# Performance work log

Hardware: AMD Instinct MI355X
Metric: run time of the kernel (lower is better)

## Reference

```python
import jax, jax.numpy as jnp
import numpy as np

NATOMS = 50000          # edge_vector rows
M = 3 * NATOMS          # attention nodes = numel(edge_vector)
NE = 1500000            # edges
NH, DH = 4, 16          # num_heads, head dim (out_dim // num_heads)


def _glorot(key, shape):
    fan_in, fan_out = shape
    lim = (6.0 / (fan_in + fan_out)) ** 0.5
    return jax.random.uniform(key, shape, jnp.float32, -lim, lim)


def setup_inputs() -> dict:
    key = jax.random.key(0)
    ks = jax.random.split(key, 12)
    inp = {
        "node_attr": jax.random.normal(ks[0], (2, M), jnp.float32),
        "edge_index": jax.random.randint(ks[1], (2, NE), 0, M, jnp.int64),
        "edge_feature": jax.random.normal(ks[2], (NE, 4), jnp.float32),
        "edge_vector": jax.random.normal(ks[3], (NATOMS, 3), jnp.float32),
        # parameters (hardcoded layer sizes in the torch module)
        "W1": _glorot(ks[4], (1, 4)),   "b1": jnp.zeros((4,), jnp.float32),
        "W2": _glorot(ks[5], (4, 16)),  "b2": jnp.zeros((16,), jnp.float32),
        "W": _glorot(ks[6], (16, 64)),  "b": jnp.zeros((64,), jnp.float32),
        "Wout": _glorot(ks[7], (64, 16)), "bout": jnp.zeros((16,), jnp.float32),
        "Wout1": _glorot(ks[8], (16, 1)), "bout1": jnp.zeros((1,), jnp.float32),
    }
    return inp


def reference(node_attr, edge_index, edge_feature, edge_vector,
              W1, b1, W2, b2, W, b, Wout, bout, Wout1, bout1):
    # node pathway: each scalar of edge_vector is one attention node
    h = edge_vector.reshape(-1, 1)                      # [M, 1]
    h = jax.nn.elu(h @ W1 + b1)                         # [M, 4]  (dropout = identity, eval)
    h = (h @ W2 + b2).reshape(-1, DH)                   # [M, 16]
    qkv = (h @ W + b).reshape(-1, NH, DH)               # [M, 4, 16]; Q==K==V (shared linear)

    # edge pathway
    e = jax.nn.elu(edge_feature @ W2 + b2)              # [Ne, 16]
    E = (e @ W + b).reshape(-1, NH, DH)                 # [Ne, 4, 16]

    src_idx = edge_index[0]
    dst_idx = edge_index[1]
    src = qkv[src_idx]                                  # K_h gather [Ne,4,16]
    dst = qkv[dst_idx]                                  # Q_h gather [Ne,4,16]
    score = (src * dst) * (1.0 / np.sqrt(DH)) * E       # edge-conditioned scores
    score = jnp.exp(jnp.clip(score.sum(-1, keepdims=True), -5.0, 5.0))  # [Ne,4,1]

    msg = qkv[src_idx] * score                          # V_h gather * score
    wV = jax.ops.segment_sum(msg, dst_idx, num_segments=M)      # [M,4,16]
    Z = jax.ops.segment_sum(score, dst_idx, num_segments=M)     # [M,4,1]

    h_out = (wV / (Z + 1e-6)).reshape(-1, NH * DH)      # [M, 64]
    h_out = jax.nn.elu(h_out @ Wout + bout)             # [M, 16]
    h_out = (h_out @ Wout1 + bout1).reshape(-1, 3)      # [M/3, 3]
    return h_out
```

## Files before the change

kernel.cpp:

```cpp
#include <hip/hip_runtime.h>
#include <hip/hip_bf16.h>
#include <cstdint>

#define DEVI __device__ __forceinline__

typedef __attribute__((ext_vector_type(8))) short bf16x8;
typedef __attribute__((ext_vector_type(4))) float f32x4;

DEVI float bf2f(unsigned short u) {
    union { unsigned int i; float f; } v; v.i = ((unsigned int)u) << 16; return v.f;
}
DEVI float ldf(const void* p, long long i, int f32) {
    return f32 ? ((const float*)p)[i] : bf2f(((const unsigned short*)p)[i]);
}
DEVI unsigned short f2bfu(float x) {
    __hip_bfloat16 h = __float2bfloat16(x);
    return *reinterpret_cast<unsigned short*>(&h);
}
DEVI short f2bf(float x) { return (short)f2bfu(x); }
DEVI float eluf(float x) { return x > 0.f ? x : __expf(x) - 1.f; }

__global__ __launch_bounds__(64) void detect_k(
    const int* __restrict__ eidx32, const unsigned int* __restrict__ wbits,
    int* __restrict__ flags)
{
    int t = threadIdx.x;
    int odd = eidx32[2 * t + 1];
    unsigned long long bz = __ballot(odd == 0);
    unsigned int w = wbits[t];
    unsigned int ex = (w >> 23) & 0xFF;
    unsigned long long bf = __ballot(ex >= 100 && ex <= 130);
    if (t == 0) {
        flags[0] = (bz == ~0ULL) ? 1 : 0;
        flags[1] = (__popcll(bf) >= 48) ? 1 : 0;
    }
}

__global__ __launch_bounds__(256) void node_qkv_k(
    const int* __restrict__ flags,
    const void* __restrict__ evec,
    const void* __restrict__ W1, const void* __restrict__ b1,
    const void* __restrict__ W2, const void* __restrict__ b2,
    const void* __restrict__ W,  const void* __restrict__ b,
    unsigned short* __restrict__ qkvb, int M_)
{
    __shared__ float sW[1024], sW2[64], sb[64], sb2[16], sW1[4], sb1[4];
    int t = threadIdx.x;
    int f32 = flags[1];
    for (int i = t; i < 1024; i += 256) sW[i] = ldf(W, i, f32);
    if (t < 64) { sW2[t] = ldf(W2, t, f32); sb[t] = ldf(b, t, f32); }
    if (t < 16) sb2[t] = ldf(b2, t, f32);
    if (t < 4)  { sW1[t] = ldf(W1, t, f32); sb1[t] = ldf(b1, t, f32); }
    __syncthreads();

    int m = blockIdx.x * 256 + t;
    if (m >= M_) return;

    float x = ldf(evec, m, f32);
    float h1[4];
    #pragma unroll
    for (int j = 0; j < 4; ++j) h1[j] = eluf(fmaf(x, sW1[j], sb1[j]));
    float h2[16];
    #pragma unroll
    for (int k = 0; k < 16; ++k) h2[k] = sb2[k];
    #pragma unroll
    for (int j = 0; j < 4; ++j)
        #pragma unroll
        for (int k = 0; k < 16; ++k) h2[k] = fmaf(h1[j], sW2[j*16 + k], h2[k]);

    uint4* op = (uint4*)(qkvb + (size_t)m * 64);
    for (int g = 0; g < 8; ++g) {
        float v[8];
        #pragma unroll
        for (int j = 0; j < 8; ++j) {
            int c = g * 8 + j;
            float a = sb[c];
            #pragma unroll
            for (int k = 0; k < 16; ++k) a = fmaf(h2[k], sW[k*64 + c], a);
            v[j] = a;
        }
        uint4 pk;
        pk.x = (unsigned)f2bfu(v[0]) | ((unsigned)f2bfu(v[1]) << 16);
        pk.y = (unsigned)f2bfu(v[2]) | ((unsigned)f2bfu(v[3]) << 16);
        pk.z = (unsigned)f2bfu(v[4]) | ((unsigned)f2bfu(v[5]) << 16);
        pk.w = (unsigned)f2bfu(v[6]) | ((unsigned)f2bfu(v[7]) << 16);
        op[g] = pk;
    }
}

__global__ __launch_bounds__(256) void hist_k(
    const int* __restrict__ flags, const int* __restrict__ eidx32,
    int* __restrict__ counts, int NE_)
{
    int e = blockIdx.x * 256 + threadIdx.x;
    if (e >= NE_) return;
    int i64 = flags[0];
    int dst = i64 ? eidx32[2LL * (NE_ + (long long)e)] : eidx32[(long long)NE_ + e];
    atomicAdd(&counts[dst], 1);
}

__global__ __launch_bounds__(256) void scan_a_k(
    const int* __restrict__ counts, int* __restrict__ bsum, int M_)
{
    __shared__ int s[256];
    int t = threadIdx.x;
    int g4 = blockIdx.x * 256 + t;
    int i0 = g4 * 4;
    int v = 0;
    if (i0 + 3 < M_) {
        int4 c = ((const int4*)counts)[g4];
        v = c.x + c.y + c.z + c.w;
    } else {
        for (int k = 0; k < 4 && i0 + k < M_; ++k) v += counts[i0 + k];
    }
    s[t] = v; __syncthreads();
    for (int off = 128; off > 0; off >>= 1) {
        if (t < off) s[t] += s[t + off];
        __syncthreads();
    }
    if (t == 0) bsum[blockIdx.x] = s[0];
}

__global__ __launch_bounds__(256) void scan_b_k(
    const int* __restrict__ bsum, int* __restrict__ bexcl, int nb,
    int* __restrict__ offsets, int M_, int NE_)
{
    __shared__ int s[256];
    int t = threadIdx.x;
    int mine = (t < nb) ? bsum[t] : 0;
    s[t] = mine; __syncthreads();
    for (int off = 1; off < 256; off <<= 1) {
        int v = (t >= off) ? s[t - off] : 0;
        __syncthreads();
        s[t] += v;
        __syncthreads();
    }
    if (t < nb) bexcl[t] = s[t] - mine;
    if (t == 0) offsets[M_] = NE_;
}

__global__ __launch_bounds__(256) void scan_c_k(
    const int* __restrict__ counts, const int* __restrict__ bexcl,
    int* __restrict__ offsets, int* __restrict__ cursor, int M_)
{
    __shared__ int s[256];
    int t = threadIdx.x;
    int g4 = blockIdx.x * 256 + t;
    int i0 = g4 * 4;
    int c0 = 0, c1 = 0, c2 = 0, c3 = 0;
    if (i0 + 3 < M_) {
        int4 c = ((const int4*)counts)[g4];
        c0 = c.x; c1 = c.y; c2 = c.z; c3 = c.w;
    } else {
        if (i0 + 0 < M_) c0 = counts[i0 + 0];
        if (i0 + 1 < M_) c1 = counts[i0 + 1];
        if (i0 + 2 < M_) c2 = counts[i0 + 2];
        if (i0 + 3 < M_) c3 = counts[i0 + 3];
    }
    int tsum = c0 + c1 + c2 + c3;
    s[t] = tsum; __syncthreads();
    for (int off = 1; off < 256; off <<= 1) {
        int v = (t >= off) ? s[t - off] : 0;
        __syncthreads();
        s[t] += v;
        __syncthreads();
    }
    int run = bexcl[blockIdx.x] + s[t] - tsum;
    if (i0 + 0 < M_) { offsets[i0+0] = run; cursor[i0+0] = run; run += c0; }
    if (i0 + 1 < M_) { offsets[i0+1] = run; cursor[i0+1] = run; run += c1; }
    if (i0 + 2 < M_) { offsets[i0+2] = run; cursor[i0+2] = run; run += c2; }
    if (i0 + 3 < M_) { offsets[i0+3] = run; cursor[i0+3] = run; run += c3; }
}

__global__ __launch_bounds__(256) void scatter_k(
    const int* __restrict__ flags, const int* __restrict__ eidx32,
    const void* __restrict__ efeat,
    int* __restrict__ cursor, int4* __restrict__ sorted, int NE_)
{
    int e = blockIdx.x * 256 + threadIdx.x;
    if (e >= NE_) return;
    int i64 = flags[0];
    int f32 = flags[1];
    int src, dst;
    if (i64) { src = eidx32[2LL * e]; dst = eidx32[2LL * (NE_ + (long long)e)]; }
    else     { src = eidx32[e];       dst = eidx32[(long long)NE_ + e]; }

    unsigned int ef01, ef23;
    if (f32) {
        const float4 f = ((const float4*)efeat)[e];
        ef01 = (unsigned)f2bfu(f.x) | ((unsigned)f2bfu(f.y) << 16);
        ef23 = (unsigned)f2bfu(f.z) | ((unsigned)f2bfu(f.w) << 16);
    } else {
        const uint2 u = ((const uint2*)efeat)[e];
        ef01 = u.x; ef23 = u.y;
    }

    int pos = atomicAdd(&cursor[dst], 1);
    sorted[pos] = make_int4(src, dst, (int)ef01, (int)ef23);
}

__global__ __launch_bounds__(256) void score_k(
    const int* __restrict__ flags, const int4* __restrict__ sorted,
    const void* __restrict__ W2, const void* __restrict__ b2,
    const void* __restrict__ W,  const void* __restrict__ b,
    const unsigned short* __restrict__ qkvb, float* __restrict__ score, int NE_)
{
    __shared__ float sW2[64], sb2[16];
    __shared__ float sE[4][16 * 68];
    int t = threadIdx.x;
    int f32 = flags[1];
    if (t < 64) sW2[t] = ldf(W2, t, f32);
    if (t < 16) sb2[t] = ldf(b2, t, f32);
    __syncthreads();

    int wv   = t >> 6;
    int lane = t & 63;
    int col  = lane & 15;
    int quad = lane >> 4;
    float* myE = &sE[wv][0];

    bf16x8 bfrag[4];
    float  bb[4];
    #pragma unroll
    for (int h = 0; h < 4; ++h) {
        #pragma unroll
        for (int jj = 0; jj < 8; ++jj) {
            int k = quad * 8 + jj;
            float wv_ = (k < 16) ? ldf(W, k * 64 + h * 16 + col, f32) : 0.f;
            bfrag[h][jj] = f2bf(wv_);
        }
        bb[h] = ldf(b, h * 16 + col, f32);
    }

    int j2 = lane >> 2, h2 = lane & 3;

    long long tiles = ((long long)NE_ + 15) >> 4;
    long long wid   = (long long)blockIdx.x * 4 + wv;
    long long nw    = (long long)gridDim.x * 4;

    for (long long tile = wid; tile < tiles; tile += nw) {
        int base = (int)(tile << 4);

        int jA = base + col;
        int4 rec = make_int4(0, 0, 0, 0);
        if (jA < NE_) rec = sorted[jA];
        float ef0 = bf2f((unsigned short)((unsigned)rec.z & 0xffff));
        float ef1 = bf2f((unsigned short)((unsigned)rec.z >> 16));
        float ef2 = bf2f((unsigned short)((unsigned)rec.w & 0xffff));
        float ef3 = bf2f((unsigned short)((unsigned)rec.w >> 16));

        bf16x8 afrag;
        #pragma unroll
        for (int jj = 0; jj < 8; ++jj) {
            int k = quad * 8 + jj;
            float v = 0.f;
            if (k < 16) {
                v = eluf(fmaf(ef0, sW2[k],
                        fmaf(ef1, sW2[16 + k],
                        fmaf(ef2, sW2[32 + k],
                        fmaf(ef3, sW2[48 + k], sb2[k])))));
            }
            afrag[jj] = f2bf(v);
        }

        f32x4 acc[4];
        #pragma unroll
        for (int h = 0; h < 4; ++h) {
            acc[h] = (f32x4){0.f, 0.f, 0.f, 0.f};
            acc[h] = __builtin_amdgcn_mfma_f32_16x16x32_bf16(afrag, bfrag[h], acc[h], 0, 0, 0);
        }

        #pragma unroll
        for (int h = 0; h < 4; ++h)
            #pragma unroll
            for (int r = 0; r < 4; ++r)
                myE[(quad * 4 + r) * 68 + h * 16 + col] = acc[h][r] + bb[h];

        asm volatile("s_waitcnt lgkmcnt(0)" ::: "memory");

        int srcj = __shfl(rec.x, j2, 64);
        int dstj = __shfl(rec.y, j2, 64);

        const uint4* sp = (const uint4*)(qkvb + (size_t)srcj * 64 + h2 * 16);
        const uint4* dp = (const uint4*)(qkvb + (size_t)dstj * 64 + h2 * 16);
        uint4 sA = sp[0], sB = sp[1], dA = dp[0], dB = dp[1];

        const float4* ep = (const float4*)(myE + j2 * 68 + h2 * 16);
        float4 e0 = ep[0], e1 = ep[1], e2 = ep[2], e3 = ep[3];
        float E[16] = {e0.x,e0.y,e0.z,e0.w, e1.x,e1.y,e1.z,e1.w,
                       e2.x,e2.y,e2.z,e2.w, e3.x,e3.y,e3.z,e3.w};

        unsigned int su[8] = {sA.x,sA.y,sA.z,sA.w, sB.x,sB.y,sB.z,sB.w};
        unsigned int du[8] = {dA.x,dA.y,dA.z,dA.w, dB.x,dB.y,dB.z,dB.w};

        float sc = 0.f;
        #pragma unroll
        for (int i = 0; i < 8; ++i) {
            float s0 = bf2f((unsigned short)(su[i] & 0xffff));
            float s1 = bf2f((unsigned short)(su[i] >> 16));
            float d0 = bf2f((unsigned short)(du[i] & 0xffff));
            float d1 = bf2f((unsigned short)(du[i] >> 16));
            sc = fmaf(s0 * d0, E[2*i],   sc);
            sc = fmaf(s1 * d1, E[2*i+1], sc);
        }
        sc *= 0.25f;
        sc = fminf(fmaxf(sc, -5.f), 5.f);
        float s = __expf(sc);

        int jW = base + j2;
        if (jW < NE_) score[(size_t)jW * 4 + h2] = s;
    }
}

__global__ __launch_bounds__(256) void accum_out_k(
    const int* __restrict__ flags,
    const int* __restrict__ offsets, const int4* __restrict__ sorted,
    const float* __restrict__ score, const unsigned short* __restrict__ qkvb,
    const void* __restrict__ Wout, const void* __restrict__ bout,
    const void* __restrict__ Wout1, const void* __restrict__ bout1,
    void* __restrict__ out, int M_)
{
    __shared__ float sWo[1024], sbo[16], sWo1[16];
    __shared__ float sbo1;
    int t = threadIdx.x;
    int f32 = flags[1];
    for (int i = t; i < 1024; i += 256) sWo[i] = ldf(Wout, i, f32);
    if (t < 16) { sbo[t] = ldf(bout, t, f32); sWo1[t] = ldf(Wout1, t, f32); }
    if (t == 0) sbo1 = ldf(bout1, 0, f32);
    __syncthreads();

    int gid = blockIdx.x * 256 + t;
    int m = gid >> 2;
    if (m >= M_) return;
    int h  = gid & 3;
    int hb = h * 16;

    int beg = offsets[m], end = offsets[m + 1];

    float acc[16];
    #pragma unroll
    for (int d = 0; d < 16; ++d) acc[d] = 0.f;
    float z = 0.f;

    int j = beg;
    for (; j + 2 <= end; j += 2) {
        int s0 = sorted[j].x;
        int s1 = sorted[j + 1].x;
        float sc0 = score[(size_t)j * 4 + h];
        float sc1 = score[(size_t)(j + 1) * 4 + h];
        const uint4* p0 = (const uint4*)(qkvb + (size_t)s0 * 64 + hb);
        const uint4* p1 = (const uint4*)(qkvb + (size_t)s1 * 64 + hb);
        uint4 a0 = p0[0], a1 = p0[1];
        uint4 b0 = p1[0], b1 = p1[1];
        z += sc0 + sc1;
        unsigned int q0[8] = {a0.x,a0.y,a0.z,a0.w, a1.x,a1.y,a1.z,a1.w};
        unsigned int q1[8] = {b0.x,b0.y,b0.z,b0.w, b1.x,b1.y,b1.z,b1.w};
        #pragma unroll
        for (int i = 0; i < 8; ++i) {
            acc[2*i]   = fmaf(bf2f((unsigned short)(q0[i] & 0xffff)), sc0, acc[2*i]);
            acc[2*i+1] = fmaf(bf2f((unsigned short)(q0[i] >> 16)),    sc0, acc[2*i+1]);
        }
        #pragma unroll
        for (int i = 0; i < 8; ++i) {
            acc[2*i]   = fmaf(bf2f((unsigned short)(q1[i] & 0xffff)), sc1, acc[2*i]);
            acc[2*i+1] = fmaf(bf2f((unsigned short)(q1[i] >> 16)),    sc1, acc[2*i+1]);
        }
    }
    if (j < end) {
        int s0 = sorted[j].x;
        float sc0 = score[(size_t)j * 4 + h];
        const uint4* p0 = (const uint4*)(qkvb + (size_t)s0 * 64 + hb);
        uint4 a0 = p0[0], a1 = p0[1];
        z += sc0;
        unsigned int q0[8] = {a0.x,a0.y,a0.z,a0.w, a1.x,a1.y,a1.z,a1.w};
        #pragma unroll
        for (int i = 0; i < 8; ++i) {
            acc[2*i]   = fmaf(bf2f((unsigned short)(q0[i] & 0xffff)), sc0, acc[2*i]);
            acc[2*i+1] = fmaf(bf2f((unsigned short)(q0[i] >> 16)),    sc0, acc[2*i+1]);
        }
    }

    float zinv = 1.f / (z + 1e-6f);

    float p[16];
    #pragma unroll
    for (int jj = 0; jj < 16; ++jj) p[jj] = 0.f;
    #pragma unroll
    for (int d = 0; d < 16; ++d) {
        float hv = acc[d] * zinv;
        #pragma unroll
        for (int jj = 0; jj < 16; ++jj) p[jj] = fmaf(hv, sWo[(hb + d) * 16 + jj], p[jj]);
    }
    #pragma unroll
    for (int jj = 0; jj < 16; ++jj) {
        p[jj] += __shfl_xor(p[jj], 1, 64);
        p[jj] += __shfl_xor(p[jj], 2, 64);
    }
    if (h == 0) {
        float o = sbo1;
        #pragma unroll
        for (int jj = 0; jj < 16; ++jj) o = fmaf(eluf(p[jj] + sbo[jj]), sWo1[jj], o);
        if (f32) ((float*)out)[m] = o;
        else     ((__hip_bfloat16*)out)[m] = __float2bfloat16(o);
    }
}

extern "C" void kernel_launch(void* const* d_in, const int* in_sizes, int n_in,
                              void* d_out, int out_size, void* d_ws, size_t ws_size,
                              hipStream_t stream)
{
    const int*  eidx  = (const int*)d_in[1];
    const void* efeat = d_in[2];
    const void* evec  = d_in[3];
    const void* W1 = d_in[4],  *b1 = d_in[5];
    const void* W2 = d_in[6],  *b2 = d_in[7];
    const void* W  = d_in[8],  *b  = d_in[9];
    const void* Wout = d_in[10], *bout = d_in[11];
    const void* Wout1 = d_in[12], *bout1 = d_in[13];

    const int M_  = in_sizes[3];
    const int NE_ = in_sizes[1] / 2;
    const int nb  = (M_ + 1023) / 1024;

    char* wp = (char*)d_ws;
    int*            flags   = (int*)wp;                 wp += 16;
    unsigned short* qkvb    = (unsigned short*)wp;      wp += (size_t)M_ * 64 * 2;
    int*            counts  = (int*)wp;                 wp += (size_t)M_ * 4;
    int*            bsum    = (int*)wp;                 wp += 2048 * 4;
    int*            bexcl   = (int*)wp;                 wp += 2048 * 4;
    int*            offsets = (int*)wp;                 wp += ((size_t)M_ + 4) * 4;
    int*            cursor  = (int*)wp;                 wp += ((size_t)M_ + 4) * 4;
    int4*           sorted  = (int4*)wp;                wp += (size_t)NE_ * 16;
    float*          scoreB  = (float*)wp;

    detect_k<<<1, 64, 0, stream>>>(eidx, (const unsigned int*)W, flags);
    hipMemsetAsync(counts, 0, (size_t)M_ * 4, stream);

    node_qkv_k<<<(M_ + 255) / 256, 256, 0, stream>>>(
        flags, evec, W1, b1, W2, b2, W, b, qkvb, M_);

    hist_k<<<(NE_ + 255) / 256, 256, 0, stream>>>(flags, eidx, counts, NE_);
    scan_a_k<<<nb, 256, 0, stream>>>(counts, bsum, M_);
    scan_b_k<<<1, 256, 0, stream>>>(bsum, bexcl, nb, offsets, M_, NE_);
    scan_c_k<<<nb, 256, 0, stream>>>(counts, bexcl, offsets, cursor, M_);
    scatter_k<<<(NE_ + 255) / 256, 256, 0, stream>>>(
        flags, eidx, efeat, cursor, sorted, NE_);

    long long tiles = ((long long)NE_ + 15) / 16;
    int sblocks = (int)((tiles + 3) / 4);
    if (sblocks > 12288) sblocks = 12288;
    score_k<<<sblocks, 256, 0, stream>>>(
        flags, sorted, W2, b2, W, b, qkvb, scoreB, NE_);

    long long tot = (long long)M_ * 4;
    accum_out_k<<<(int)((tot + 255) / 256), 256, 0, stream>>>(
        flags, offsets, sorted, scoreB, qkvb,
        Wout, bout, Wout1, bout1, d_out, M_);
}
```

Before: 423.8 us.

## Fuse edge score computation with per-node aggregation and output MLP

Merges the score kernel and the accumulate/output kernel into one. Each wavefront owns 16 consecutive destination nodes and walks their contiguous sorted edge range in chunks of 16. Scores and source indices are staged in shared memory and consumed immediately, so the global score buffer write and read-back go away. In exchange, each wave's work depends on its nodes' degrees, which can cause load imbalance. The inner accumulation loop is also serial per edge and the shared memory footprint per block grows.

```diff
diff --git a/kernel.cpp b/kernel.cpp
--- a/kernel.cpp
+++ b/kernel.cpp
@@ -199,25 +199,38 @@
     sorted[pos] = make_int4(src, dst, (int)ef01, (int)ef23);
 }
 
-__global__ __launch_bounds__(256) void score_k(
-    const int* __restrict__ flags, const int4* __restrict__ sorted,
+__global__ __launch_bounds__(256) void fused_k(
+    const int* __restrict__ flags,
+    const int* __restrict__ offsets, const int4* __restrict__ sorted,
     const void* __restrict__ W2, const void* __restrict__ b2,
     const void* __restrict__ W,  const void* __restrict__ b,
-    const unsigned short* __restrict__ qkvb, float* __restrict__ score, int NE_)
+    const unsigned short* __restrict__ qkvb,
+    const void* __restrict__ Wout, const void* __restrict__ bout,
+    const void* __restrict__ Wout1, const void* __restrict__ bout1,
+    void* __restrict__ out, int M_)
 {
     __shared__ float sW2[64], sb2[16];
+    __shared__ float sWo[1024], sbo[16], sWo1[16];
+    __shared__ float sbo1;
     __shared__ float sE[4][16 * 68];
+    __shared__ float sS[4][64];
+    __shared__ int   sSrc[4][16];
+
     int t = threadIdx.x;
     int f32 = flags[1];
+    for (int i = t; i < 1024; i += 256) sWo[i] = ldf(Wout, i, f32);
     if (t < 64) sW2[t] = ldf(W2, t, f32);
-    if (t < 16) sb2[t] = ldf(b2, t, f32);
+    if (t < 16) { sb2[t] = ldf(b2, t, f32); sbo[t] = ldf(bout, t, f32); sWo1[t] = ldf(Wout1, t, f32); }
+    if (t == 0) sbo1 = ldf(bout1, 0, f32);
     __syncthreads();
 
-    int wv   = t >> 6;
+    int wvi  = t >> 6;
     int lane = t & 63;
     int col  = lane & 15;
     int quad = lane >> 4;
-    float* myE = &sE[wv][0];
+    float* myE  = &sE[wvi][0];
+    float* myS  = &sS[wvi][0];
+    int*   mySrc = &sSrc[wvi][0];
 
     bf16x8 bfrag[4];
     float  bb[4];
@@ -232,18 +245,26 @@
         bb[h] = ldf(b, h * 16 + col, f32);
     }
 
+    int m0 = (blockIdx.x * 4 + wvi) * 16;
+    if (m0 >= M_) return;
+    int mtop = m0 + 16; if (mtop > M_) mtop = M_;
+    int beg = offsets[m0], end = offsets[mtop];
+
     int j2 = lane >> 2, h2 = lane & 3;
-
-    long long tiles = ((long long)NE_ + 15) >> 4;
-    long long wid   = (long long)blockIdx.x * 4 + wv;
-    long long nw    = (long long)gridDim.x * 4;
-
-    for (long long tile = wid; tile < tiles; tile += nw) {
-        int base = (int)(tile << 4);
-
-        int jA = base + col;
+    int m = m0 + j2;
+    bool valid = (m < M_);
+    int sbm = valid ? offsets[m]     : 0;
+    int sem = valid ? offsets[m + 1] : 0;
+
+    float acc[16];
+    #pragma unroll
+    for (int d = 0; d < 16; ++d) acc[d] = 0.f;
+    float z = 0.f;
+
+    for (int c = beg; c < end; c += 16) {
+        int jA = c + col;
         int4 rec = make_int4(0, 0, 0, 0);
-        if (jA < NE_) rec = sorted[jA];
+        if (jA < end) rec = sorted[jA];
         float ef0 = bf2f((unsigned short)((unsigned)rec.z & 0xffff));
         float ef1 = bf2f((unsigned short)((unsigned)rec.z >> 16));
         float ef2 = bf2f((unsigned short)((unsigned)rec.w & 0xffff));
@@ -263,24 +284,23 @@
             afrag[jj] = f2bf(v);
         }
 
-        f32x4 acc[4];
+        f32x4 a4[4];
         #pragma unroll
         for (int h = 0; h < 4; ++h) {
-            acc[h] = (f32x4){0.f, 0.f, 0.f, 0.f};
-            acc[h] = __builtin_amdgcn_mfma_f32_16x16x32_bf16(afrag, bfrag[h], acc[h], 0, 0, 0);
+            a4[h] = (f32x4){0.f, 0.f, 0.f, 0.f};
+            a4[h] = __builtin_amdgcn_mfma_f32_16x16x32_bf16(afrag, bfrag[h], a4[h], 0, 0, 0);
         }
 
         #pragma unroll
         for (int h = 0; h < 4; ++h)
             #pragma unroll
             for (int r = 0; r < 4; ++r)
-                myE[(quad * 4 + r) * 68 + h * 16 + col] = acc[h][r] + bb[h];
-
+                myE[(quad * 4 + r) * 68 + h * 16 + col] = a4[h][r] + bb[h];
+        if (lane < 16) mySrc[col] = rec.x;
         asm volatile("s_waitcnt lgkmcnt(0)" ::: "memory");
 
         int srcj = __shfl(rec.x, j2, 64);
         int dstj = __shfl(rec.y, j2, 64);
-
         const uint4* sp = (const uint4*)(qkvb + (size_t)srcj * 64 + h2 * 16);
         const uint4* dp = (const uint4*)(qkvb + (size_t)dstj * 64 + h2 * 16);
         uint4 sA = sp[0], sB = sp[1], dA = dp[0], dB = dp[1];
@@ -289,7 +309,6 @@
         float4 e0 = ep[0], e1 = ep[1], e2 = ep[2], e3 = ep[3];
         float E[16] = {e0.x,e0.y,e0.z,e0.w, e1.x,e1.y,e1.z,e1.w,
                        e2.x,e2.y,e2.z,e2.w, e3.x,e3.y,e3.z,e3.w};
-
         unsigned int su[8] = {sA.x,sA.y,sA.z,sA.w, sB.x,sB.y,sB.z,sB.w};
         unsigned int du[8] = {dA.x,dA.y,dA.z,dA.w, dB.x,dB.y,dB.z,dB.w};
 
@@ -305,83 +324,30 @@
         }
         sc *= 0.25f;
         sc = fminf(fmaxf(sc, -5.f), 5.f);
-        float s = __expf(sc);
-
-        int jW = base + j2;
-        if (jW < NE_) score[(size_t)jW * 4 + h2] = s;
-    }
-}
-
-__global__ __launch_bounds__(256) void accum_out_k(
-    const int* __restrict__ flags,
-    const int* __restrict__ offsets, const int4* __restrict__ sorted,
-    const float* __restrict__ score, const unsigned short* __restrict__ qkvb,
-    const void* __restrict__ Wout, const void* __restrict__ bout,
-    const void* __restrict__ Wout1, const void* __restrict__ bout1,
-    void* __restrict__ out, int M_)
-{
-    __shared__ float sWo[1024], sbo[16], sWo1[16];
-    __shared__ float sbo1;
-    int t = threadIdx.x;
-    int f32 = flags[1];
-    for (int i = t; i < 1024; i += 256) sWo[i] = ldf(Wout, i, f32);
-    if (t < 16) { sbo[t] = ldf(bout, t, f32); sWo1[t] = ldf(Wout1, t, f32); }
-    if (t == 0) sbo1 = ldf(bout1, 0, f32);
-    __syncthreads();
-
-    int gid = blockIdx.x * 256 + t;
-    int m = gid >> 2;
-    if (m >= M_) return;
-    int h  = gid & 3;
-    int hb = h * 16;
-
-    int beg = offsets[m], end = offsets[m + 1];
-
-    float acc[16];
-    #pragma unroll
-    for (int d = 0; d < 16; ++d) acc[d] = 0.f;
-    float z = 0.f;
-
-    int j = beg;
-    for (; j + 2 <= end; j += 2) {
-        int s0 = sorted[j].x;
-        int s1 = sorted[j + 1].x;
-        float sc0 = score[(size_t)j * 4 + h];
-        float sc1 = score[(size_t)(j + 1) * 4 + h];
-        const uint4* p0 = (const uint4*)(qkvb + (size_t)s0 * 64 + hb);
-        const uint4* p1 = (const uint4*)(qkvb + (size_t)s1 * 64 + hb);
-        uint4 a0 = p0[0], a1 = p0[1];
-        uint4 b0 = p1[0], b1 = p1[1];
-        z += sc0 + sc1;
-        unsigned int q0[8] = {a0.x,a0.y,a0.z,a0.w, a1.x,a1.y,a1.z,a1.w};
-        unsigned int q1[8] = {b0.x,b0.y,b0.z,b0.w, b1.x,b1.y,b1.z,b1.w};
-        #pragma unroll
-        for (int i = 0; i < 8; ++i) {
-            acc[2*i]   = fmaf(bf2f((unsigned short)(q0[i] & 0xffff)), sc0, acc[2*i]);
-            acc[2*i+1] = fmaf(bf2f((unsigned short)(q0[i] >> 16)),    sc0, acc[2*i+1]);
-        }
-        #pragma unroll
-        for (int i = 0; i < 8; ++i) {
-            acc[2*i]   = fmaf(bf2f((unsigned short)(q1[i] & 0xffff)), sc1, acc[2*i]);
-            acc[2*i+1] = fmaf(bf2f((unsigned short)(q1[i] >> 16)),    sc1, acc[2*i+1]);
-        }
-    }
-    if (j < end) {
-        int s0 = sorted[j].x;
-        float sc0 = score[(size_t)j * 4 + h];
-        const uint4* p0 = (const uint4*)(qkvb + (size_t)s0 * 64 + hb);
-        uint4 a0 = p0[0], a1 = p0[1];
-        z += sc0;
-        unsigned int q0[8] = {a0.x,a0.y,a0.z,a0.w, a1.x,a1.y,a1.z,a1.w};
-        #pragma unroll
-        for (int i = 0; i < 8; ++i) {
-            acc[2*i]   = fmaf(bf2f((unsigned short)(q0[i] & 0xffff)), sc0, acc[2*i]);
-            acc[2*i+1] = fmaf(bf2f((unsigned short)(q0[i] >> 16)),    sc0, acc[2*i+1]);
-        }
-    }
+        myS[j2 * 4 + h2] = __expf(sc);
+        asm volatile("s_waitcnt lgkmcnt(0)" ::: "memory");
+
+        int lo = sbm - c; if (lo < 0) lo = 0;
+        int hi = sem - c; if (hi > 16) hi = 16;
+        for (int jj = lo; jj < hi; ++jj) {
+            float s = myS[jj * 4 + h2];
+            int srcm = mySrc[jj];
+            const uint4* p = (const uint4*)(qkvb + (size_t)srcm * 64 + h2 * 16);
+            uint4 a0 = p[0], a1 = p[1];
+            z += s;
+            unsigned int q[8] = {a0.x,a0.y,a0.z,a0.w, a1.x,a1.y,a1.z,a1.w};
+            #pragma unroll
+            for (int i = 0; i < 8; ++i) {
+                acc[2*i]   = fmaf(bf2f((unsigned short)(q[i] & 0xffff)), s, acc[2*i]);
+                acc[2*i+1] = fmaf(bf2f((unsigned short)(q[i] >> 16)),    s, acc[2*i+1]);
+            }
+        }
+    }
+
+    if (!valid) return;
 
     float zinv = 1.f / (z + 1e-6f);
-
+    int hb = h2 * 16;
     float p[16];
     #pragma unroll
     for (int jj = 0; jj < 16; ++jj) p[jj] = 0.f;
@@ -396,7 +362,7 @@
         p[jj] += __shfl_xor(p[jj], 1, 64);
         p[jj] += __shfl_xor(p[jj], 2, 64);
     }
-    if (h == 0) {
+    if (h2 == 0) {
         float o = sbo1;
         #pragma unroll
         for (int jj = 0; jj < 16; ++jj) o = fmaf(eluf(p[jj] + sbo[jj]), sWo1[jj], o);
@@ -430,8 +396,7 @@
     int*            bexcl   = (int*)wp;                 wp += 2048 * 4;
     int*            offsets = (int*)wp;                 wp += ((size_t)M_ + 4) * 4;
     int*            cursor  = (int*)wp;                 wp += ((size_t)M_ + 4) * 4;
-    int4*           sorted  = (int4*)wp;                wp += (size_t)NE_ * 16;
-    float*          scoreB  = (float*)wp;
+    int4*           sorted  = (int4*)wp;
 
     detect_k<<<1, 64, 0, stream>>>(eidx, (const unsigned int*)W, flags);
     hipMemsetAsync(counts, 0, (size_t)M_ * 4, stream);
@@ -446,14 +411,8 @@
     scatter_k<<<(NE_ + 255) / 256, 256, 0, stream>>>(
         flags, eidx, efeat, cursor, sorted, NE_);
 
-    long long tiles = ((long long)NE_ + 15) / 16;
-    int sblocks = (int)((tiles + 3) / 4);
-    if (sblocks > 12288) sblocks = 12288;
-    score_k<<<sblocks, 256, 0, stream>>>(
-        flags, sorted, W2, b2, W, b, qkvb, scoreB, NE_);
-
-    long long tot = (long long)M_ * 4;
-    accum_out_k<<<(int)((tot + 255) / 256), 256, 0, stream>>>(
-        flags, offsets, sorted, scoreB, qkvb,
+    int fblocks = (M_ + 63) / 64;
+    fused_k<<<fblocks, 256, 0, stream>>>(
+        flags, offsets, sorted, W2, b2, W, b, qkvb,
         Wout, bout, Wout1, bout1, d_out, M_);
 }
```

New measurement: 452.0 us. 1.07x slower.

## Split edge scatter into coarse bucket pass and local placement pass

Applied to the files above, without the earlier changes.

Replaces the single random scatter of edges by destination with two passes. The first groups edges into buckets of 128 destination nodes, using one atomic cursor per bucket. The second reads the staging array in bucket order and places each edge at its exact slot, so its writes land in a small region. The aim is better write locality and cache behaviour during the counting sort, at the cost of an extra kernel launch, an extra pass over 1.5M 16-byte records, and heavier atomic contention on the bucket cursors. The score buffer now reuses the staging memory.

```diff
diff --git a/kernel.cpp b/kernel.cpp
--- a/kernel.cpp
+++ b/kernel.cpp
@@ -172,10 +172,17 @@
     if (i0 + 3 < M_) { offsets[i0+3] = run; cursor[i0+3] = run; run += c3; }
 }
 
-__global__ __launch_bounds__(256) void scatter_k(
+__global__ __launch_bounds__(256) void binit_k(
+    const int* __restrict__ offsets, int* __restrict__ bcur, int NB)
+{
+    int b = blockIdx.x * 256 + threadIdx.x;
+    if (b < NB) bcur[b] = offsets[b * 128];
+}
+
+__global__ __launch_bounds__(256) void bucket_k(
     const int* __restrict__ flags, const int* __restrict__ eidx32,
     const void* __restrict__ efeat,
-    int* __restrict__ cursor, int4* __restrict__ sorted, int NE_)
+    int* __restrict__ bcur, int4* __restrict__ staging, int NE_)
 {
     int e = blockIdx.x * 256 + threadIdx.x;
     if (e >= NE_) return;
@@ -195,8 +202,19 @@
         ef01 = u.x; ef23 = u.y;
     }
 
-    int pos = atomicAdd(&cursor[dst], 1);
-    sorted[pos] = make_int4(src, dst, (int)ef01, (int)ef23);
+    int pos = atomicAdd(&bcur[dst >> 7], 1);
+    staging[pos] = make_int4(src, dst, (int)ef01, (int)ef23);
+}
+
+__global__ __launch_bounds__(256) void place_k(
+    const int4* __restrict__ staging, int* __restrict__ cursor,
+    int4* __restrict__ sorted, int NE_)
+{
+    int j = blockIdx.x * 256 + threadIdx.x;
+    if (j >= NE_) return;
+    int4 r = staging[j];
+    int pos = atomicAdd(&cursor[r.y], 1);
+    sorted[pos] = r;
 }
 
 __global__ __launch_bounds__(256) void score_k(
@@ -421,6 +439,7 @@
     const int M_  = in_sizes[3];
     const int NE_ = in_sizes[1] / 2;
     const int nb  = (M_ + 1023) / 1024;
+    const int NB  = (M_ + 127) / 128;
 
     char* wp = (char*)d_ws;
     int*            flags   = (int*)wp;                 wp += 16;
@@ -430,8 +449,13 @@
     int*            bexcl   = (int*)wp;                 wp += 2048 * 4;
     int*            offsets = (int*)wp;                 wp += ((size_t)M_ + 4) * 4;
     int*            cursor  = (int*)wp;                 wp += ((size_t)M_ + 4) * 4;
+    int*            bcur    = (int*)wp;                 wp += ((size_t)NB + 4) * 4;
+    wp = (char*)(((uintptr_t)wp + 15) & ~(uintptr_t)15);
     int4*           sorted  = (int4*)wp;                wp += (size_t)NE_ * 16;
+    int4*           staging = (int4*)wp;                wp += (size_t)NE_ * 16;
     float*          scoreB  = (float*)wp;
+
+    scoreB = (float*)staging;
 
     detect_k<<<1, 64, 0, stream>>>(eidx, (const unsigned int*)W, flags);
     hipMemsetAsync(counts, 0, (size_t)M_ * 4, stream);
@@ -443,8 +467,12 @@
     scan_a_k<<<nb, 256, 0, stream>>>(counts, bsum, M_);
     scan_b_k<<<1, 256, 0, stream>>>(bsum, bexcl, nb, offsets, M_, NE_);
     scan_c_k<<<nb, 256, 0, stream>>>(counts, bexcl, offsets, cursor, M_);
-    scatter_k<<<(NE_ + 255) / 256, 256, 0, stream>>>(
-        flags, eidx, efeat, cursor, sorted, NE_);
+    binit_k<<<(NB + 255) / 256, 256, 0, stream>>>(offsets, bcur, NB);
+
+    bucket_k<<<(NE_ + 255) / 256, 256, 0, stream>>>(
+        flags, eidx, efeat, bcur, staging, NE_);
+    place_k<<<(NE_ + 255) / 256, 256, 0, stream>>>(
+        staging, cursor, sorted, NE_);
 
     long long tiles = ((long long)NE_ + 15) / 16;
     int sblocks = (int)((tiles + 3) / 4);
```

Measured after the change: 655.1 us. 54.6% more time.

## Record per-edge rank in histogram to drop atomics from scatter pass

Applied to the files above, without the earlier changes.

The histogram kernel now keeps the value returned by each atomicAdd as a per-edge rank and handles four edges per thread with vectorized index loads. The scatter kernel computes each edge's position as offsets[dst] + rank, so it no longer needs a second round of atomics on a cursor array. The cursor array and its writes in the scan kernel are removed. In exchange, a new rank array of NE ints is written and read back, and the order of edges within each segment now follows the histogram pass rather than the scatter pass.

```diff
diff --git a/kernel.cpp b/kernel.cpp
--- a/kernel.cpp
+++ b/kernel.cpp
@@ -90,13 +90,33 @@
 
 __global__ __launch_bounds__(256) void hist_k(
     const int* __restrict__ flags, const int* __restrict__ eidx32,
-    int* __restrict__ counts, int NE_)
-{
-    int e = blockIdx.x * 256 + threadIdx.x;
-    if (e >= NE_) return;
+    int* __restrict__ counts, int* __restrict__ rank, int NE_)
+{
+    int e0 = (blockIdx.x * 256 + threadIdx.x) * 4;
+    if (e0 >= NE_) return;
     int i64 = flags[0];
-    int dst = i64 ? eidx32[2LL * (NE_ + (long long)e)] : eidx32[(long long)NE_ + e];
-    atomicAdd(&counts[dst], 1);
+    if (e0 + 3 < NE_) {
+        int d[4];
+        if (i64) {
+            long long w = 2LL * (NE_ + (long long)e0);
+            int4 a = *(const int4*)(eidx32 + w);
+            int4 b = *(const int4*)(eidx32 + w + 4);
+            d[0] = a.x; d[1] = a.z; d[2] = b.x; d[3] = b.z;
+        } else {
+            #pragma unroll
+            for (int i = 0; i < 4; ++i) d[i] = eidx32[(long long)NE_ + e0 + i];
+        }
+        int r[4];
+        #pragma unroll
+        for (int i = 0; i < 4; ++i) r[i] = atomicAdd(&counts[d[i]], 1);
+        *(int4*)(rank + e0) = make_int4(r[0], r[1], r[2], r[3]);
+    } else {
+        for (int e = e0; e < NE_; ++e) {
+            int dst = i64 ? eidx32[2LL * (NE_ + (long long)e)]
+                          : eidx32[(long long)NE_ + e];
+            rank[e] = atomicAdd(&counts[dst], 1);
+        }
+    }
 }
 
 __global__ __launch_bounds__(256) void scan_a_k(
@@ -141,7 +161,7 @@
 
 __global__ __launch_bounds__(256) void scan_c_k(
     const int* __restrict__ counts, const int* __restrict__ bexcl,
-    int* __restrict__ offsets, int* __restrict__ cursor, int M_)
+    int* __restrict__ offsets, int M_)
 {
     __shared__ int s[256];
     int t = threadIdx.x;
@@ -166,16 +186,17 @@
         __syncthreads();
     }
     int run = bexcl[blockIdx.x] + s[t] - tsum;
-    if (i0 + 0 < M_) { offsets[i0+0] = run; cursor[i0+0] = run; run += c0; }
-    if (i0 + 1 < M_) { offsets[i0+1] = run; cursor[i0+1] = run; run += c1; }
-    if (i0 + 2 < M_) { offsets[i0+2] = run; cursor[i0+2] = run; run += c2; }
-    if (i0 + 3 < M_) { offsets[i0+3] = run; cursor[i0+3] = run; run += c3; }
+    if (i0 + 0 < M_) { offsets[i0+0] = run; run += c0; }
+    if (i0 + 1 < M_) { offsets[i0+1] = run; run += c1; }
+    if (i0 + 2 < M_) { offsets[i0+2] = run; run += c2; }
+    if (i0 + 3 < M_) { offsets[i0+3] = run; run += c3; }
 }
 
 __global__ __launch_bounds__(256) void scatter_k(
     const int* __restrict__ flags, const int* __restrict__ eidx32,
     const void* __restrict__ efeat,
-    int* __restrict__ cursor, int4* __restrict__ sorted, int NE_)
+    const int* __restrict__ offsets, const int* __restrict__ rank,
+    int4* __restrict__ sorted, int NE_)
 {
     int e = blockIdx.x * 256 + threadIdx.x;
     if (e >= NE_) return;
@@ -195,7 +216,7 @@
         ef01 = u.x; ef23 = u.y;
     }
 
-    int pos = atomicAdd(&cursor[dst], 1);
+    int pos = offsets[dst] + rank[e];
     sorted[pos] = make_int4(src, dst, (int)ef01, (int)ef23);
 }
 
@@ -429,22 +450,24 @@
     int*            bsum    = (int*)wp;                 wp += 2048 * 4;
     int*            bexcl   = (int*)wp;                 wp += 2048 * 4;
     int*            offsets = (int*)wp;                 wp += ((size_t)M_ + 4) * 4;
-    int*            cursor  = (int*)wp;                 wp += ((size_t)M_ + 4) * 4;
+    int*            rank    = (int*)wp;                 wp += (size_t)NE_ * 4;
+    wp = (char*)(((uintptr_t)wp + 15) & ~(uintptr_t)15);
     int4*           sorted  = (int4*)wp;                wp += (size_t)NE_ * 16;
     float*          scoreB  = (float*)wp;
 
     detect_k<<<1, 64, 0, stream>>>(eidx, (const unsigned int*)W, flags);
-    hipMemsetAsync(counts, 0, (size_t)M_ * 4, stream);
+    (void)hipMemsetAsync(counts, 0, (size_t)M_ * 4, stream);
 
     node_qkv_k<<<(M_ + 255) / 256, 256, 0, stream>>>(
         flags, evec, W1, b1, W2, b2, W, b, qkvb, M_);
 
-    hist_k<<<(NE_ + 255) / 256, 256, 0, stream>>>(flags, eidx, counts, NE_);
+    int q4 = (NE_ + 3) / 4;
+    hist_k<<<(q4 + 255) / 256, 256, 0, stream>>>(flags, eidx, counts, rank, NE_);
     scan_a_k<<<nb, 256, 0, stream>>>(counts, bsum, M_);
     scan_b_k<<<1, 256, 0, stream>>>(bsum, bexcl, nb, offsets, M_, NE_);
-    scan_c_k<<<nb, 256, 0, stream>>>(counts, bexcl, offsets, cursor, M_);
+    scan_c_k<<<nb, 256, 0, stream>>>(counts, bexcl, offsets, M_);
     scatter_k<<<(NE_ + 255) / 256, 256, 0, stream>>>(
-        flags, eidx, efeat, cursor, sorted, NE_);
+        flags, eidx, efeat, offsets, rank, sorted, NE_);
 
     long long tiles = ((long long)NE_ + 15) / 16;
     int sblocks = (int)((tiles + 3) / 4);
```

Result: faster. 366.0 us (-13.6%).
